# Kernel tuning notes

Hardware: AMD Instinct MI355X
Metric: run time of the kernel (lower is better)

Reference implementation:

```python
import jax, jax.numpy as jnp
import numpy as np

ALPHA = 0.2  # LeakyReLU negative slope
NEG = -9e15  # mask value from original code


def setup_inputs() -> dict:
    key = jax.random.key(0)
    k1, k2, k3, k4 = jax.random.split(key, 4)
    N, F_in, F_out = 8192, 256, 128
    h = jax.random.normal(k1, (N, F_in), dtype=jnp.float32)
    adj = jax.random.randint(k2, (N, N), 0, 2, dtype=jnp.int32)
    # xavier-ish scaled params
    W = jax.random.normal(k3, (F_out, F_in), dtype=jnp.float32) * (1.0 / np.sqrt(F_in))
    a = jax.random.normal(k4, (1, 2 * F_out), dtype=jnp.float32) * (1.0 / np.sqrt(2 * F_out))
    return {"h": h, "adj": adj, "W": W, "a": a}


def reference(h, adj, W, a):
    # Wh: [N, F_out]
    Wh = h @ W.T
    F_out = Wh.shape[1]
    # Algebraic decomposition of the pairwise-concat score:
    # e[i,j] = leakyrelu(a . [Wh_i ; Wh_j]) = leakyrelu(f1_i + f2_j)
    a1 = a[0, :F_out]   # [F_out]
    a2 = a[0, F_out:]   # [F_out]
    f1 = Wh @ a1        # [N]
    f2 = Wh @ a2        # [N]
    e = jax.nn.leaky_relu(f1[:, None] + f2[None, :], negative_slope=ALPHA)  # [N, N]
    scores = jnp.where(adj > 0, e, NEG)
    attention = jax.nn.softmax(scores, axis=1)  # dropout omitted (eval mode)
    return attention @ Wh  # [N, F_out]
```

## Files before the change

kernel.cpp:

```cpp
#include <hip/hip_runtime.h>
#include <hip/hip_bf16.h>


typedef __bf16 bf16;
typedef __attribute__((ext_vector_type(8))) __bf16 bf16x8;
typedef __attribute__((ext_vector_type(4))) float f32x4;

#define NN 8192
#define F_IN 256
#define F_OUT 128
#define LOG2E 1.44269504088896f
#define ALPHA 0.2f
#define KSLICES 8

__device__ __forceinline__ void split8(const float* __restrict__ p,
                                       bf16x8& hi, bf16x8& lo) {
    const float4 u = *(const float4*)p;
    const float4 v = *(const float4*)(p + 4);
    float f[8] = {u.x, u.y, u.z, u.w, v.x, v.y, v.z, v.w};
#pragma unroll
    for (int j = 0; j < 8; ++j) {
        const bf16 h = (bf16)f[j];
        hi[j] = h;
        lo[j] = (bf16)(f[j] - (float)h);
    }
}

__global__ __launch_bounds__(128) void gat_wh(const float* __restrict__ h,
                                              const float* __restrict__ W,
                                              const float* __restrict__ a,
                                              bf16* __restrict__ WhT,
                                              float* __restrict__ f1L,
                                              float* __restrict__ f2L) {
    const int tid = threadIdx.x;
    const int wv = tid >> 6;
    const int l15 = tid & 15;
    const int g = (tid & 63) >> 4;
    const int rowbase = blockIdx.x * 32 + wv * 16;

    f32x4 acc[8];
    const f32x4 zz = {0.f, 0.f, 0.f, 0.f};
#pragma unroll
    for (int nf = 0; nf < 8; ++nf) acc[nf] = zz;

#pragma unroll
    for (int ks = 0; ks < 8; ++ks) {
        const int k = ks * 32 + g * 8;
        bf16x8 ah, al;
        split8(h + (size_t)(rowbase + l15) * F_IN + k, ah, al);
#pragma unroll
        for (int nf = 0; nf < 8; ++nf) {
            bf16x8 bh, bl;
            split8(W + (size_t)(nf * 16 + l15) * F_IN + k, bh, bl);
            acc[nf] = __builtin_amdgcn_mfma_f32_16x16x32_bf16(ah, bh, acc[nf], 0, 0, 0);
            acc[nf] = __builtin_amdgcn_mfma_f32_16x16x32_bf16(ah, bl, acc[nf], 0, 0, 0);
            acc[nf] = __builtin_amdgcn_mfma_f32_16x16x32_bf16(al, bh, acc[nf], 0, 0, 0);
        }
    }

#pragma unroll
    for (int nf = 0; nf < 8; ++nf)
#pragma unroll
        for (int r = 0; r < 4; ++r)
            WhT[(size_t)(nf * 16 + l15) * NN + rowbase + g * 4 + r] = (bf16)acc[nf][r];

    float a1c[8], a2c[8];
#pragma unroll
    for (int nf = 0; nf < 8; ++nf) {
        a1c[nf] = a[nf * 16 + l15];
        a2c[nf] = a[F_OUT + nf * 16 + l15];
    }
#pragma unroll
    for (int r = 0; r < 4; ++r) {
        float s1 = 0.f, s2 = 0.f;
#pragma unroll
        for (int nf = 0; nf < 8; ++nf) {
            s1 += acc[nf][r] * a1c[nf];
            s2 += acc[nf][r] * a2c[nf];
        }
        s1 += __shfl_xor(s1, 1, 16);
        s1 += __shfl_xor(s1, 2, 16);
        s1 += __shfl_xor(s1, 4, 16);
        s1 += __shfl_xor(s1, 8, 16);
        s2 += __shfl_xor(s2, 1, 16);
        s2 += __shfl_xor(s2, 2, 16);
        s2 += __shfl_xor(s2, 4, 16);
        s2 += __shfl_xor(s2, 8, 16);
        if (l15 == 0) {
            f1L[rowbase + g * 4 + r] = s1 * LOG2E;
            f2L[rowbase + g * 4 + r] = s2 * LOG2E;
        }
    }
}

__global__ __launch_bounds__(512, 4) void gat_flash7(
        const int* __restrict__ adj,
        const bf16* __restrict__ WhT,
        const float* __restrict__ f1L,
        const float* __restrict__ f2L,
        float* __restrict__ O_part,
        float* __restrict__ rs_part) {
    __shared__ __align__(16) char lds[45568];
#define MOFF 32768
#define FOFF 41472

    const int tid = threadIdx.x;
    const int wv = tid >> 6;
    const int l = tid & 63;
    const int l15 = l & 15;
    const int g = l >> 4;
    const int half = l >> 5;
    const int lane32 = l & 31;
    const int rb = blockIdx.x >> 3;
    const int ks = blockIdx.x & 7;
    const int row0 = rb * 128;
    const int lrow = wv * 16 + l15;

    const float f1a = f1L[row0 + lrow];

    f32x4 acc[8];
    const f32x4 zz = {0.f, 0.f, 0.f, 0.f};
#pragma unroll
    for (int nf = 0; nf < 8; ++nf) acc[nf] = zz;
    float rs0 = 0.f;

    {
        const float2 v = *(const float2*)(f2L + ks * 1024 + tid * 2);
        *(float2*)(lds + FOFF + tid * 8) = v;
    }

    for (int su = 0; su < 2; ++su) {
        __syncthreads();
#pragma unroll
        for (int i = 0; i < 8; ++i) {
            const int lr = wv * 16 + 2 * i + half;
            const int* ap = adj + (size_t)(row0 + lr) * NN + ks * 1024 + su * 512 + lane32 * 4;
#pragma unroll
            for (int p = 0; p < 4; ++p) {
                const int4 v = *(const int4*)(ap + p * 128);
                const unsigned int n = (v.x > 0 ? 1u : 0u) | (v.y > 0 ? 2u : 0u) |
                                       (v.z > 0 ? 4u : 0u) | (v.w > 0 ? 8u : 0u);
                const unsigned int o = __shfl_xor(n, 1);
                if ((l & 1) == 0)
                    *(unsigned char*)(lds + MOFF + lr * 68 + p * 16 + (lane32 >> 1)) =
                        (unsigned char)(n | (o << 4));
            }
        }

#pragma unroll
        for (int bc = 0; bc < 4; ++bc) {
            __syncthreads();
            const int kg = ks * 1024 + su * 512 + bc * 128;
#pragma unroll
            for (int j = 0; j < 4; ++j) {
                const int u = j * 512 + tid;
                const int cc = u >> 4;
                const int ku = u & 15;
                const bf16x8 v = *(const bf16x8*)(WhT + (size_t)cc * NN + kg + ku * 8);
                *(bf16x8*)(lds + ((cc * 256 + ku * 16) ^ ((cc & 7) << 4))) = v;
            }
            __syncthreads();

#pragma unroll
            for (int s = 0; s < 4; ++s) {
                const int t = bc * 4 + s;
                const int tt = su * 16 + t;
                const unsigned int mb =
                    *(const unsigned char*)(lds + MOFF + lrow * 68 + t * 4 + g);
                const float4 fa = *(const float4*)(lds + FOFF + tt * 128 + g * 32);
                const float4 fb = *(const float4*)(lds + FOFF + tt * 128 + g * 32 + 16);
                const float ff[8] = {fa.x, fa.y, fa.z, fa.w, fb.x, fb.y, fb.z, fb.w};

                bf16x8 pa;
#pragma unroll
                for (int j = 0; j < 8; ++j) {
                    const float x = f1a + ff[j];
                    const float e = __builtin_amdgcn_exp2f(fmaxf(x, ALPHA * x));
                    pa[j] = (bf16)((mb & (1u << j)) ? e : 0.f);
                }
#pragma unroll
                for (int j = 0; j < 8; ++j) rs0 += (float)pa[j];

                __builtin_amdgcn_s_setprio(1);
#pragma unroll
                for (int nf = 0; nf < 8; ++nf) {
                    const int c = nf * 16 + l15;
                    const bf16x8 bh = *(const bf16x8*)(
                        lds + ((c * 256 + s * 64 + g * 16) ^ ((c & 7) << 4)));
                    acc[nf] =
                        __builtin_amdgcn_mfma_f32_16x16x32_bf16(pa, bh, acc[nf], 0, 0, 0);
                }
                __builtin_amdgcn_s_setprio(0);
            }
        }
    }

    rs0 += __shfl_xor(rs0, 16);
    rs0 += __shfl_xor(rs0, 32);
    if (l < 16) rs_part[(size_t)ks * NN + row0 + lrow] = rs0;

    float* accL = (float*)lds;
#pragma unroll
    for (int hh = 0; hh < 2; ++hh) {
        __syncthreads();
        if ((wv >> 2) == hh) {
            const int rbase = (wv & 3) * 16;
#pragma unroll
            for (int nf = 0; nf < 8; ++nf)
#pragma unroll
                for (int r = 0; r < 4; ++r)
                    accL[(rbase + g * 4 + r) * 132 + nf * 16 + l15] = acc[nf][r];
        }
        __syncthreads();
        const int rr = tid >> 3;
        const int seg = tid & 7;
        float* dst = O_part + ((size_t)ks << 20) +
                     (size_t)(row0 + hh * 64 + rr) * F_OUT + seg * 16;
        const float* src = accL + rr * 132 + seg * 16;
        *(float4*)(dst + 0) = *(const float4*)(src + 0);
        *(float4*)(dst + 4) = *(const float4*)(src + 4);
        *(float4*)(dst + 8) = *(const float4*)(src + 8);
        *(float4*)(dst + 12) = *(const float4*)(src + 12);
    }
#undef MOFF
#undef FOFF
}

__global__ __launch_bounds__(256) void gat_reduce(const float* __restrict__ O_part,
                                                  const float* __restrict__ rs_part,
                                                  float* __restrict__ out) {
    const int idx = blockIdx.x * 256 + threadIdx.x;
    const int r = idx >> 5;
    const int c = (idx & 31) * 4;
    float rsum = 0.f;
#pragma unroll
    for (int s = 0; s < KSLICES; ++s) rsum += rs_part[(size_t)s * NN + r];
    float4 o = {0.f, 0.f, 0.f, 0.f};
#pragma unroll
    for (int s = 0; s < KSLICES; ++s) {
        const float4 v =
            *(const float4*)(O_part + ((size_t)s << 20) + (size_t)r * F_OUT + c);
        o.x += v.x;
        o.y += v.y;
        o.z += v.z;
        o.w += v.w;
    }
    const float inv = 1.0f / rsum;
    o.x *= inv;
    o.y *= inv;
    o.z *= inv;
    o.w *= inv;
    *(float4*)(out + (size_t)r * F_OUT + c) = o;
}

extern "C" void kernel_launch(void* const* d_in, const int* in_sizes, int n_in,
                              void* d_out, int out_size, void* d_ws, size_t ws_size,
                              hipStream_t stream) {
    const float* h = (const float*)d_in[0];
    const int* adj = (const int*)d_in[1];
    const float* W = (const float*)d_in[2];
    const float* a = (const float*)d_in[3];
    float* out = (float*)d_out;

    char* ws = (char*)d_ws;
    const size_t MB = 1024 * 1024;
    bf16* WhT = (bf16*)ws;
    float* f1L = (float*)(ws + 2 * MB);
    float* f2L = f1L + NN;
    float* rs_part = (float*)(ws + 3 * MB);
    float* O_part = (float*)(ws + 4 * MB);

    gat_wh<<<256, 128, 0, stream>>>(h, W, a, WhT, f1L, f2L);
    gat_flash7<<<512, 512, 0, stream>>>(adj, WhT, f1L, f2L, O_part, rs_part);
    gat_reduce<<<NN * F_OUT / 4 / 256, 256, 0, stream>>>(O_part, rs_part, out);
}
```

Before: 123.4 us.

## Software-pipeline adjacency loads into registers across 128-column windows

Restructures the flash kernel's main loop into eight 128-column windows. The adjacency ints for the next window are prefetched into registers while the current window computes, then packed into a double-buffered LDS bitmask after the MFMAs. This is meant to hide the large adj read latency (the dominant HBM traffic) behind compute instead of stalling at the start of each 512-column chunk. It adds 32 int4 registers of pressure per thread and swaps __syncthreads for a manual waitcnt plus barrier, which could hurt occupancy or correctness if vmcnt is not handled.

```diff
diff --git a/kernel.cpp b/kernel.cpp
--- a/kernel.cpp
+++ b/kernel.cpp
@@ -93,16 +93,37 @@
     }
 }
 
-__global__ __launch_bounds__(512, 4) void gat_flash7(
+#define MOFF(P) (32768 + (P) * 2560)
+#define FOFF 37888
+
+#define LOADW(W)                                                                 \
+    do {                                                                         \
+        const int* ap_ = adj + (size_t)(row0 + wv * 16 + half) * NN + kbase +    \
+                         (W) * 128 + lane32 * 4;                                 \
+        _Pragma("unroll") for (int i = 0; i < 8; ++i)                            \
+            A[i] = *(const int4*)(ap_ + (size_t)(2 * i) * NN);                   \
+    } while (0)
+
+#define PACKW(P)                                                                 \
+    do {                                                                         \
+        _Pragma("unroll") for (int i = 0; i < 8; ++i) {                          \
+            const unsigned int n_ = (A[i].x > 0 ? 1u : 0u) | (A[i].y > 0 ? 2u : 0u) | \
+                                    (A[i].z > 0 ? 4u : 0u) | (A[i].w > 0 ? 8u : 0u);  \
+            const unsigned int o_ = __shfl_xor(n_, 1);                           \
+            if ((l & 1) == 0)                                                    \
+                *(unsigned char*)(lds + MOFF(P) + (wv * 16 + 2 * i + half) * 20 + \
+                                  (lane32 >> 1)) = (unsigned char)(n_ | (o_ << 4)); \
+        }                                                                        \
+    } while (0)
+
+__global__ __launch_bounds__(512, 4) void gat_flash8(
         const int* __restrict__ adj,
         const bf16* __restrict__ WhT,
         const float* __restrict__ f1L,
         const float* __restrict__ f2L,
         float* __restrict__ O_part,
         float* __restrict__ rs_part) {
-    __shared__ __align__(16) char lds[45568];
-#define MOFF 32768
-#define FOFF 41472
+    __shared__ __align__(16) char lds[41984];
 
     const int tid = threadIdx.x;
     const int wv = tid >> 6;
@@ -114,6 +135,7 @@
     const int rb = blockIdx.x >> 3;
     const int ks = blockIdx.x & 7;
     const int row0 = rb * 128;
+    const int kbase = ks * 1024;
     const int lrow = wv * 16 + l15;
 
     const float f1a = f1L[row0 + lrow];
@@ -125,74 +147,66 @@
     float rs0 = 0.f;
 
     {
-        const float2 v = *(const float2*)(f2L + ks * 1024 + tid * 2);
+        const float2 v = *(const float2*)(f2L + kbase + tid * 2);
         *(float2*)(lds + FOFF + tid * 8) = v;
     }
 
-    for (int su = 0; su < 2; ++su) {
-        __syncthreads();
-#pragma unroll
-        for (int i = 0; i < 8; ++i) {
-            const int lr = wv * 16 + 2 * i + half;
-            const int* ap = adj + (size_t)(row0 + lr) * NN + ks * 1024 + su * 512 + lane32 * 4;
-#pragma unroll
-            for (int p = 0; p < 4; ++p) {
-                const int4 v = *(const int4*)(ap + p * 128);
-                const unsigned int n = (v.x > 0 ? 1u : 0u) | (v.y > 0 ? 2u : 0u) |
-                                       (v.z > 0 ? 4u : 0u) | (v.w > 0 ? 8u : 0u);
-                const unsigned int o = __shfl_xor(n, 1);
-                if ((l & 1) == 0)
-                    *(unsigned char*)(lds + MOFF + lr * 68 + p * 16 + (lane32 >> 1)) =
-                        (unsigned char)(n | (o << 4));
+    int4 A[8];
+    LOADW(0);
+    PACKW(0);
+
+    for (int w = 0; w < 8; ++w) {
+        asm volatile("s_waitcnt lgkmcnt(0)" ::: "memory");
+        __builtin_amdgcn_s_barrier();
+        __builtin_amdgcn_sched_barrier(0);
+
+        if (w < 7) LOADW(w + 1);
+
+#pragma unroll
+        for (int j = 0; j < 4; ++j) {
+            const int u = j * 512 + tid;
+            const int cc = u >> 4;
+            const int ku = u & 15;
+            const bf16x8 v =
+                *(const bf16x8*)(WhT + (size_t)cc * NN + kbase + w * 128 + ku * 8);
+            *(bf16x8*)(lds + ((cc * 256 + ku * 16) ^ ((cc & 7) << 4))) = v;
+        }
+
+        asm volatile("s_waitcnt lgkmcnt(0)" ::: "memory");
+        __builtin_amdgcn_s_barrier();
+        __builtin_amdgcn_sched_barrier(0);
+
+#pragma unroll
+        for (int s = 0; s < 4; ++s) {
+            const int tt = w * 4 + s;
+            const unsigned int mb =
+                *(const unsigned char*)(lds + MOFF(w & 1) + lrow * 20 + s * 4 + g);
+            const float4 fa = *(const float4*)(lds + FOFF + tt * 128 + g * 32);
+            const float4 fb = *(const float4*)(lds + FOFF + tt * 128 + g * 32 + 16);
+            const float ff[8] = {fa.x, fa.y, fa.z, fa.w, fb.x, fb.y, fb.z, fb.w};
+
+            bf16x8 pa;
+#pragma unroll
+            for (int j = 0; j < 8; ++j) {
+                const float x = f1a + ff[j];
+                const float e = __builtin_amdgcn_exp2f(fmaxf(x, ALPHA * x));
+                pa[j] = (bf16)((mb & (1u << j)) ? e : 0.f);
             }
-        }
-
-#pragma unroll
-        for (int bc = 0; bc < 4; ++bc) {
-            __syncthreads();
-            const int kg = ks * 1024 + su * 512 + bc * 128;
-#pragma unroll
-            for (int j = 0; j < 4; ++j) {
-                const int u = j * 512 + tid;
-                const int cc = u >> 4;
-                const int ku = u & 15;
-                const bf16x8 v = *(const bf16x8*)(WhT + (size_t)cc * NN + kg + ku * 8);
-                *(bf16x8*)(lds + ((cc * 256 + ku * 16) ^ ((cc & 7) << 4))) = v;
+#pragma unroll
+            for (int j = 0; j < 8; ++j) rs0 += (float)pa[j];
+
+            __builtin_amdgcn_s_setprio(1);
+#pragma unroll
+            for (int nf = 0; nf < 8; ++nf) {
+                const int c = nf * 16 + l15;
+                const bf16x8 bh = *(const bf16x8*)(
+                    lds + ((c * 256 + s * 64 + g * 16) ^ ((c & 7) << 4)));
+                acc[nf] = __builtin_amdgcn_mfma_f32_16x16x32_bf16(pa, bh, acc[nf], 0, 0, 0);
             }
-            __syncthreads();
-
-#pragma unroll
-            for (int s = 0; s < 4; ++s) {
-                const int t = bc * 4 + s;
-                const int tt = su * 16 + t;
-                const unsigned int mb =
-                    *(const unsigned char*)(lds + MOFF + lrow * 68 + t * 4 + g);
-                const float4 fa = *(const float4*)(lds + FOFF + tt * 128 + g * 32);
-                const float4 fb = *(const float4*)(lds + FOFF + tt * 128 + g * 32 + 16);
-                const float ff[8] = {fa.x, fa.y, fa.z, fa.w, fb.x, fb.y, fb.z, fb.w};
-
-                bf16x8 pa;
-#pragma unroll
-                for (int j = 0; j < 8; ++j) {
-                    const float x = f1a + ff[j];
-                    const float e = __builtin_amdgcn_exp2f(fmaxf(x, ALPHA * x));
-                    pa[j] = (bf16)((mb & (1u << j)) ? e : 0.f);
-                }
-#pragma unroll
-                for (int j = 0; j < 8; ++j) rs0 += (float)pa[j];
-
-                __builtin_amdgcn_s_setprio(1);
-#pragma unroll
-                for (int nf = 0; nf < 8; ++nf) {
-                    const int c = nf * 16 + l15;
-                    const bf16x8 bh = *(const bf16x8*)(
-                        lds + ((c * 256 + s * 64 + g * 16) ^ ((c & 7) << 4)));
-                    acc[nf] =
-                        __builtin_amdgcn_mfma_f32_16x16x32_bf16(pa, bh, acc[nf], 0, 0, 0);
-                }
-                __builtin_amdgcn_s_setprio(0);
-            }
-        }
+            __builtin_amdgcn_s_setprio(0);
+        }
+
+        if (w < 7) PACKW((w + 1) & 1);
     }
 
     rs0 += __shfl_xor(rs0, 16);
@@ -222,8 +236,6 @@
         *(float4*)(dst + 8) = *(const float4*)(src + 8);
         *(float4*)(dst + 12) = *(const float4*)(src + 12);
     }
-#undef MOFF
-#undef FOFF
 }
 
 __global__ __launch_bounds__(256) void gat_reduce(const float* __restrict__ O_part,
@@ -271,6 +283,6 @@
     float* O_part = (float*)(ws + 4 * MB);
 
     gat_wh<<<256, 128, 0, stream>>>(h, W, a, WhT, f1L, f2L);
-    gat_flash7<<<512, 512, 0, stream>>>(adj, WhT, f1L, f2L, O_part, rs_part);
+    gat_flash8<<<512, 512, 0, stream>>>(adj, WhT, f1L, f2L, O_part, rs_part);
     gat_reduce<<<NN * F_OUT / 4 / 256, 256, 0, stream>>>(O_part, rs_part, out);
 }
```

Result: slower. 161.5 us (+30.8%).
